# Kernel optimization log

Hardware: AMD Instinct MI355X
Metric: run time of the kernel (lower is better)

The kernel has to match this reference:

```python
import jax, jax.numpy as jnp
import numpy as np

B, I, HID, H, KS = 64, 1024, 2048, 8, 4
D = HID // H  # head_size = 256; also BlockDiagonal block size = (2*I)//H = 256
EPS = 1e-5


def setup_inputs() -> dict:
    key = jax.random.key(0)
    ks = jax.random.split(key, 16)
    r = lambda i, shape, s=0.02: jax.random.normal(ks[i], shape, dtype=jnp.float32) * s
    z = lambda shape: jnp.zeros(shape, jnp.float32)
    return {
        "x": jax.random.normal(ks[0], (B, I), dtype=jnp.float32),
        "h_prev": z((B, H, D)),
        "c_prev": z((B, H, D, D)),
        "n_prev": z((B, H, D)),
        "m_prev": z((B, H)),
        "ln_w": jnp.ones((I,), jnp.float32), "ln_b": z((I,)),
        "W_ul": r(1, (I, HID)), "b_ul": z((HID,)),
        "W_ur": r(2, (I, HID)), "b_ur": z((HID,)),
        "W_conv": r(3, (HID, HID, KS)), "b_conv": z((HID,)),
        "W_skip": r(4, (HID, HID)), "b_skip": z((HID,)),
        "W_q": r(5, (H, D, D)), "b_q": z((HID,)),
        "W_k": r(6, (H, D, D)), "b_k": z((HID,)),
        "W_v": r(7, (H, D, D)), "b_v": z((HID,)),
        "W_i": r(8, (HID, H)), "b_i": z((H,)),
        "W_f": r(9, (HID, H)), "b_f": z((H,)),
        "W_o": r(10, (HID, HID)), "b_o": z((HID,)),
        "W_down": r(11, (HID, I)), "b_down": z((I,)),
        "gn_w": jnp.ones((HID,), jnp.float32), "gn_b": z((HID,)),
    }


def _block_diag(zf, W, b):
    # BlockDiagonal: chunk last dim into H blocks, per-block Linear, concat -> [B,H,D]
    zh = zf.reshape(zf.shape[0], H, -1)
    return jnp.einsum('bhi,hio->bho', zh, W) + b.reshape(H, -1)


def reference(x, h_prev, c_prev, n_prev, m_prev, ln_w, ln_b, W_ul, b_ul, W_ur, b_ur,
              W_conv, b_conv, W_skip, b_skip, W_q, b_q, W_k, b_k, W_v, b_v,
              W_i, b_i, W_f, b_f, W_o, b_o, W_down, b_down, gn_w, gn_b):
    # LayerNorm
    mu = x.mean(-1, keepdims=True)
    var = jnp.mean((x - mu) ** 2, -1, keepdims=True)
    xn = (x - mu) * jax.lax.rsqrt(var + EPS) * ln_w + ln_b
    # Up projections
    xl = xn @ W_ul + b_ul            # [B, 2I] == [B, HID]
    xr = xn @ W_ur + b_ur
    # Causal conv over a length-1 sequence: after left padding + slicing, only the
    # last kernel tap (index KS-1) touches real data -> linear map with W_conv[:,:,KS-1]
    xc = jax.nn.silu(xl @ W_conv[:, :, KS - 1].T + b_conv)
    x_skip = xc @ W_skip + b_skip    # [B, HID]
    q = _block_diag(xc, W_q, b_q)                       # [B,H,D]
    k = _block_diag(xc, W_k, b_k) / jnp.sqrt(jnp.float32(D))
    v = _block_diag(xl, W_v, b_v)
    i_t = xc @ W_i + b_i             # [B,H]
    f_t = xc @ W_f + b_f
    o = jax.nn.sigmoid(xl @ W_o + b_o).reshape(-1, H, D)
    # Stabilized exponential gating
    m_t = jnp.maximum(f_t + m_prev, i_t)
    i_g = jnp.exp(i_t - m_t)
    f_g = jnp.exp(f_t + m_prev - m_t)
    # Outer-product state update + bilinear readout
    c_t = f_g[..., None, None] * c_prev + i_g[..., None, None] * jnp.einsum('bhd,bhk->bhdk', v, k)
    n_t = f_g[..., None] * n_prev + i_g[..., None] * k
    num = jnp.einsum('bhdk,bhk->bhd', c_t, q)
    den = jnp.clip(jnp.einsum('bhd,bhd->bh', n_t, q), 1.0, None)[..., None]
    h_t = o * num / den              # [B,H,D]
    # GroupNorm with num_groups == num_heads: normalize per head
    g_mu = h_t.mean(-1, keepdims=True)
    g_var = jnp.mean((h_t - g_mu) ** 2, -1, keepdims=True)
    gn = ((h_t - g_mu) * jax.lax.rsqrt(g_var + EPS)).reshape(-1, HID) * gn_w + gn_b
    out = (gn + x_skip) * jax.nn.silu(xr)
    out = out @ W_down + b_down
    final = out + x
    return (final, h_t, c_t, n_t, m_t)
```

## Files before the change

kernel.cpp:

```cpp
#include <hip/hip_runtime.h>
#include <cstddef>

typedef __bf16 bf16;
typedef __bf16 bf16x8 __attribute__((ext_vector_type(8)));
typedef short  s16x8  __attribute__((ext_vector_type(8)));
typedef float  f32x4  __attribute__((ext_vector_type(4)));

template <class T> T&& declv() noexcept;
template <class, class = void> struct takes_bf16vec { static constexpr bool value = false; };
template <class V> struct takes_bf16vec<V, decltype((void)__builtin_amdgcn_mfma_f32_16x16x32_bf16(
    declv<V>(), declv<V>(), declv<f32x4>(), 0, 0, 0))> { static constexpr bool value = true; };

template <class V>
__device__ __forceinline__ f32x4 mfma_bf16_16x16x32(V a, V b, f32x4 c) {
  if constexpr (takes_bf16vec<V>::value) {
    return __builtin_amdgcn_mfma_f32_16x16x32_bf16(a, b, c, 0, 0, 0);
  } else {
    return __builtin_amdgcn_mfma_f32_16x16x32_bf16(
        __builtin_bit_cast(s16x8, a), __builtin_bit_cast(s16x8, b), c, 0, 0, 0);
  }
}

constexpr int M_NONE = 0, M_SILU = 1, M_SIG = 2, M_SCALE = 3, M_FINAL = 4;
constexpr int FLAG_BD = 1, FLAG_S4 = 2;

__global__ __launch_bounds__(256) void ln_kernel(const float* __restrict__ x,
                                                 const float* __restrict__ w,
                                                 const float* __restrict__ bs,
                                                 bf16* __restrict__ xn) {
  const int b = blockIdx.x, tid = threadIdx.x;
  __shared__ float red[256];
  float vals[4];
  float s = 0.f;
#pragma unroll
  for (int i = 0; i < 4; ++i) { vals[i] = x[b * 1024 + i * 256 + tid]; s += vals[i]; }
  red[tid] = s; __syncthreads();
  for (int off = 128; off; off >>= 1) { if (tid < off) red[tid] += red[tid + off]; __syncthreads(); }
  const float mu = red[0] * (1.f / 1024.f);
  __syncthreads();
  float s2 = 0.f;
#pragma unroll
  for (int i = 0; i < 4; ++i) { const float d = vals[i] - mu; s2 += d * d; }
  red[tid] = s2; __syncthreads();
  for (int off = 128; off; off >>= 1) { if (tid < off) red[tid] += red[tid + off]; __syncthreads(); }
  const float rs = rsqrtf(red[0] * (1.f / 1024.f) + 1e-5f);
#pragma unroll
  for (int i = 0; i < 4; ++i) {
    const int j = i * 256 + tid;
    xn[b * 1024 + j] = (bf16)((vals[i] - mu) * rs * w[j] + bs[j]);
  }
}

__global__ __launch_bounds__(256) void gemm_sk(
    const bf16* __restrict__ A, const float* __restrict__ W,
    const float* __restrict__ bias, const float* __restrict__ xadd,
    float* __restrict__ outF, bf16* __restrict__ outB,
    int K, int N, int ldA, int mode, int flags) {
  const int tid = threadIdx.x;
  const int lane = tid & 63, wave = tid >> 6;
  const int l15 = lane & 15, quad = lane >> 4;
  const int n0 = blockIdx.x << 4;
  const bool bd = (flags & FLAG_BD) != 0, s4 = (flags & FLAG_S4) != 0;

  int Keff = K, aCol0 = 0, ldB = N, wn0 = n0;
  const float* Wb = W;
  if (bd) {
    const int h = n0 >> 8;
    Keff = 256; aCol0 = h << 8; Wb = W + (size_t)h * 65536; ldB = 256; wn0 = n0 & 255;
  }
  const int kchunk = Keff >> 2;
  const int kbeg = wave * kchunk, kend = kbeg + kchunk;

  f32x4 acc0{}, acc1{}, acc2{}, acc3{};
  for (int k = kbeg; k < kend; k += 32) {
    const int kk = k + quad * 8;
    bf16x8 bfrag;
    if (s4) {
      const float* wp = W + ((size_t)(wn0 + l15) * 2048 + kk) * 4 + 3;
#pragma unroll
      for (int j = 0; j < 8; ++j) bfrag[j] = (bf16)wp[j * 4];
    } else {
      const float* wp = Wb + (size_t)kk * ldB + wn0 + l15;
#pragma unroll
      for (int j = 0; j < 8; ++j) bfrag[j] = (bf16)wp[(size_t)j * ldB];
    }
    const bf16* ap = A + (size_t)l15 * ldA + aCol0 + kk;
    const size_t st = (size_t)16 * ldA;
    bf16x8 a0 = *(const bf16x8*)(ap);
    bf16x8 a1 = *(const bf16x8*)(ap + st);
    bf16x8 a2 = *(const bf16x8*)(ap + 2 * st);
    bf16x8 a3 = *(const bf16x8*)(ap + 3 * st);
    acc0 = mfma_bf16_16x16x32(a0, bfrag, acc0);
    acc1 = mfma_bf16_16x16x32(a1, bfrag, acc1);
    acc2 = mfma_bf16_16x16x32(a2, bfrag, acc2);
    acc3 = mfma_bf16_16x16x32(a3, bfrag, acc3);
  }
  __shared__ float lds[4][64][20];
#pragma unroll
  for (int r = 0; r < 4; ++r) {
    const int rr = quad * 4 + r;
    lds[wave][rr][l15]      = acc0[r];
    lds[wave][16 + rr][l15] = acc1[r];
    lds[wave][32 + rr][l15] = acc2[r];
    lds[wave][48 + rr][l15] = acc3[r];
  }
  __syncthreads();
  const int col = tid & 15, rb = (tid >> 4) << 2;
  const float bv = bias[n0 + col];
#pragma unroll
  for (int r2 = 0; r2 < 4; ++r2) {
    const int row = rb + r2;
    float v = lds[0][row][col] + lds[1][row][col] + lds[2][row][col] + lds[3][row][col] + bv;
    if (mode == M_SILU)       v = v / (1.f + expf(-v));
    else if (mode == M_SIG)   v = 1.f / (1.f + expf(-v));
    else if (mode == M_SCALE) v *= 0.0625f;
    else if (mode == M_FINAL) v += xadd[(size_t)row * N + n0 + col];
    const size_t oi = (size_t)row * N + n0 + col;
    if (outF) outF[oi] = v;
    if (outB) outB[oi] = (bf16)v;
  }
}

__global__ __launch_bounds__(256) void gates_kernel(
    const bf16* __restrict__ xc, const float* __restrict__ Wi, const float* __restrict__ bi,
    const float* __restrict__ Wf, const float* __restrict__ bfv, const float* __restrict__ m_prev,
    float* __restrict__ ig, float* __restrict__ fg, float* __restrict__ mt_out) {
  const int b = blockIdx.x, tid = threadIdx.x;
  float ai[8] = {}, af[8] = {};
  for (int k = tid; k < 2048; k += 256) {
    const float xv = (float)xc[b * 2048 + k];
    const float4 wi0 = *(const float4*)(Wi + (size_t)k * 8);
    const float4 wi1 = *(const float4*)(Wi + (size_t)k * 8 + 4);
    const float4 wf0 = *(const float4*)(Wf + (size_t)k * 8);
    const float4 wf1 = *(const float4*)(Wf + (size_t)k * 8 + 4);
    ai[0] += xv * wi0.x; ai[1] += xv * wi0.y; ai[2] += xv * wi0.z; ai[3] += xv * wi0.w;
    ai[4] += xv * wi1.x; ai[5] += xv * wi1.y; ai[6] += xv * wi1.z; ai[7] += xv * wi1.w;
    af[0] += xv * wf0.x; af[1] += xv * wf0.y; af[2] += xv * wf0.z; af[3] += xv * wf0.w;
    af[4] += xv * wf1.x; af[5] += xv * wf1.y; af[6] += xv * wf1.z; af[7] += xv * wf1.w;
  }
  __shared__ float ri[256][8], rf[256][8];
#pragma unroll
  for (int h = 0; h < 8; ++h) { ri[tid][h] = ai[h]; rf[tid][h] = af[h]; }
  __syncthreads();
  for (int off = 128; off; off >>= 1) {
    if (tid < off) {
#pragma unroll
      for (int h = 0; h < 8; ++h) { ri[tid][h] += ri[tid + off][h]; rf[tid][h] += rf[tid + off][h]; }
    }
    __syncthreads();
  }
  if (tid < 8) {
    const float it = ri[0][tid] + bi[tid];
    const float ft = rf[0][tid] + bfv[tid];
    const float mp = m_prev[b * 8 + tid];
    const float mt = fmaxf(ft + mp, it);
    mt_out[b * 8 + tid] = mt;
    ig[b * 8 + tid] = expf(it - mt);
    fg[b * 8 + tid] = expf(ft + mp - mt);
  }
}

__global__ __launch_bounds__(256) void state_kernel(
    const float* __restrict__ c_prev, const float* __restrict__ n_prev,
    const float* __restrict__ qf, const float* __restrict__ kf,
    const float* __restrict__ vf, const float* __restrict__ of,
    const float* __restrict__ ig, const float* __restrict__ fg,
    const float* __restrict__ xskip, const float* __restrict__ xrf,
    const float* __restrict__ gnw, const float* __restrict__ gnb,
    float* __restrict__ ct_out, float* __restrict__ nt_out,
    float* __restrict__ ht_out, bf16* __restrict__ pre_bf) {
  const int bh = blockIdx.x, b = bh >> 3, h = bh & 7;
  const int tid = threadIdx.x, lane = tid & 63, wave = tid >> 6;
  const int vb = b * 2048 + h * 256;

  __shared__ float q_s[256], k_s[256], v_s[256], num_s[256], red[256];

  const float i_g = ig[bh], f_g = fg[bh];
  const float kv = kf[vb + tid], qv = qf[vb + tid];
  q_s[tid] = qv; k_s[tid] = kv; v_s[tid] = vf[vb + tid];
  const float nv = f_g * n_prev[bh * 256 + tid] + i_g * kv;
  nt_out[bh * 256 + tid] = nv;
  red[tid] = nv * qv;
  __syncthreads();
  for (int off = 128; off; off >>= 1) { if (tid < off) red[tid] += red[tid + off]; __syncthreads(); }
  const float den = fmaxf(red[0], 1.0f);

  const size_t cb = (size_t)bh << 16;
  const int c0 = lane << 2;
  const float qx = q_s[c0], qy = q_s[c0 + 1], qz = q_s[c0 + 2], qw = q_s[c0 + 3];
  const float kx = k_s[c0], ky = k_s[c0 + 1], kz = k_s[c0 + 2], kw = k_s[c0 + 3];
  for (int r = 0; r < 64; ++r) {
    const int row = (wave << 6) + r;
    const float vd = v_s[row];
    const size_t off = cb + ((size_t)row << 8) + c0;
    const float4 cp = *(const float4*)(c_prev + off);
    float4 cn;
    cn.x = f_g * cp.x + i_g * kx * vd;
    cn.y = f_g * cp.y + i_g * ky * vd;
    cn.z = f_g * cp.z + i_g * kz * vd;
    cn.w = f_g * cp.w + i_g * kw * vd;
    *(float4*)(ct_out + off) = cn;
    float p = cn.x * qx + cn.y * qy + cn.z * qz + cn.w * qw;
#pragma unroll
    for (int m = 32; m; m >>= 1) p += __shfl_xor(p, m, 64);
    if (lane == 0) num_s[row] = p;
  }
  __syncthreads();

  const float num = num_s[tid];
  const float hv = of[vb + tid] * num / den;
  ht_out[bh * 256 + tid] = hv;

  __syncthreads();
  red[tid] = hv; __syncthreads();
  for (int off = 128; off; off >>= 1) { if (tid < off) red[tid] += red[tid + off]; __syncthreads(); }
  const float mu = red[0] * (1.f / 256.f);
  __syncthreads();
  const float dv = hv - mu;
  red[tid] = dv * dv; __syncthreads();
  for (int off = 128; off; off >>= 1) { if (tid < off) red[tid] += red[tid + off]; __syncthreads(); }
  const float gn = (hv - mu) * rsqrtf(red[0] * (1.f / 256.f) + 1e-5f);

  const int j = h * 256 + tid;
  const float xr = xrf[b * 2048 + j];
  const float pre = (gn * gnw[j] + gnb[j] + xskip[b * 2048 + j]) * (xr / (1.f + expf(-xr)));
  pre_bf[b * 2048 + j] = (bf16)pre;
}

extern "C" void kernel_launch(void* const* d_in, const int* in_sizes, int n_in,
                              void* d_out, int out_size, void* d_ws, size_t ws_size,
                              hipStream_t stream) {
  (void)in_sizes; (void)n_in; (void)out_size; (void)ws_size;
  const float* x      = (const float*)d_in[0];
  const float* c_prev = (const float*)d_in[2];
  const float* n_prev = (const float*)d_in[3];
  const float* m_prev = (const float*)d_in[4];
  const float* ln_w = (const float*)d_in[5];
  const float* ln_b = (const float*)d_in[6];
  const float* W_ul = (const float*)d_in[7];
  const float* b_ul = (const float*)d_in[8];
  const float* W_ur = (const float*)d_in[9];
  const float* b_ur = (const float*)d_in[10];
  const float* W_conv = (const float*)d_in[11];
  const float* b_conv = (const float*)d_in[12];
  const float* W_skip = (const float*)d_in[13];
  const float* b_skip = (const float*)d_in[14];
  const float* W_q = (const float*)d_in[15];
  const float* b_q = (const float*)d_in[16];
  const float* W_k = (const float*)d_in[17];
  const float* b_k = (const float*)d_in[18];
  const float* W_v = (const float*)d_in[19];
  const float* b_v = (const float*)d_in[20];
  const float* W_i = (const float*)d_in[21];
  const float* b_i = (const float*)d_in[22];
  const float* W_f = (const float*)d_in[23];
  const float* b_f = (const float*)d_in[24];
  const float* W_o = (const float*)d_in[25];
  const float* b_o = (const float*)d_in[26];
  const float* W_down = (const float*)d_in[27];
  const float* b_down = (const float*)d_in[28];
  const float* gn_w = (const float*)d_in[29];
  const float* gn_b = (const float*)d_in[30];

  float* out_final = (float*)d_out;
  float* out_ht = out_final + 65536;
  float* out_ct = out_final + 196608;
  float* out_nt = out_final + 33751040;
  float* out_mt = out_final + 33882112;

  char* ws = (char*)d_ws;
  bf16*  xn_bf   = (bf16*)(ws + 0);
  bf16*  xl_bf   = (bf16*)(ws + 131072);
  bf16*  xc_bf   = (bf16*)(ws + 393216);
  bf16*  pre_bf  = (bf16*)(ws + 655360);
  float* xr_f    = (float*)(ws + 917504);
  float* xskip_f = (float*)(ws + 1441792);
  float* q_f     = (float*)(ws + 1966080);
  float* k_f     = (float*)(ws + 2490368);
  float* v_f     = (float*)(ws + 3014656);
  float* o_f     = (float*)(ws + 3538944);
  float* ig_f    = (float*)(ws + 4063232);
  float* fg_f    = (float*)(ws + 4065280);

  ln_kernel<<<64, 256, 0, stream>>>(x, ln_w, ln_b, xn_bf);
  gemm_sk<<<128, 256, 0, stream>>>(xn_bf, W_ul, b_ul, nullptr, nullptr, xl_bf, 1024, 2048, 1024, M_NONE, 0);
  gemm_sk<<<128, 256, 0, stream>>>(xn_bf, W_ur, b_ur, nullptr, xr_f, nullptr, 1024, 2048, 1024, M_NONE, 0);
  gemm_sk<<<128, 256, 0, stream>>>(xl_bf, W_conv, b_conv, nullptr, nullptr, xc_bf, 2048, 2048, 2048, M_SILU, FLAG_S4);
  gemm_sk<<<128, 256, 0, stream>>>(xc_bf, W_skip, b_skip, nullptr, xskip_f, nullptr, 2048, 2048, 2048, M_NONE, 0);
  gemm_sk<<<128, 256, 0, stream>>>(xc_bf, W_q, b_q, nullptr, q_f, nullptr, 256, 2048, 2048, M_NONE, FLAG_BD);
  gemm_sk<<<128, 256, 0, stream>>>(xc_bf, W_k, b_k, nullptr, k_f, nullptr, 256, 2048, 2048, M_SCALE, FLAG_BD);
  gemm_sk<<<128, 256, 0, stream>>>(xl_bf, W_v, b_v, nullptr, v_f, nullptr, 256, 2048, 2048, M_NONE, FLAG_BD);
  gemm_sk<<<128, 256, 0, stream>>>(xl_bf, W_o, b_o, nullptr, o_f, nullptr, 2048, 2048, 2048, M_SIG, 0);
  gates_kernel<<<64, 256, 0, stream>>>(xc_bf, W_i, b_i, W_f, b_f, m_prev, ig_f, fg_f, out_mt);
  state_kernel<<<512, 256, 0, stream>>>(c_prev, n_prev, q_f, k_f, v_f, o_f, ig_f, fg_f,
                                        xskip_f, xr_f, gn_w, gn_b, out_ct, out_nt, out_ht, pre_bf);
  gemm_sk<<<64, 256, 0, stream>>>(pre_bf, W_down, b_down, x, out_final, nullptr, 2048, 1024, 2048, M_FINAL, 0);
}
```

Measured before the change: 521.8 us.

## Split-K GEMMs with combine kernels, merge paired projections, split state update

Projection GEMMs now use split-K with templated compile-time sizes, writing partial sums that a separate combine kernel reduces and then applies bias and activation. Paired GEMMs that share inputs (ul/ur, skip/o) are merged into one launch, and the q/k/v block-diagonal GEMMs are fused into a single launch. The state update is split into a kernel with 4096 blocks that streams c_prev and a second kernel for normalization, which raises parallelism beyond the earlier 128 or 512 blocks. Output buffers (c_t and h_t) are reused as scratch for the partial sums, and the extra launches and partial-sum traffic add cost.

Result: faster. 448.8 us (-14.0%).

```diff
diff --git a/kernel.cpp b/kernel.cpp
--- a/kernel.cpp
+++ b/kernel.cpp
@@ -22,7 +22,6 @@
 }
 
 constexpr int M_NONE = 0, M_SILU = 1, M_SIG = 2, M_SCALE = 3, M_FINAL = 4;
-constexpr int FLAG_BD = 1, FLAG_S4 = 2;
 
 __global__ __launch_bounds__(256) void ln_kernel(const float* __restrict__ x,
                                                  const float* __restrict__ w,
@@ -51,40 +50,46 @@
   }
 }
 
-__global__ __launch_bounds__(256) void gemm_sk(
-    const bf16* __restrict__ A, const float* __restrict__ W,
-    const float* __restrict__ bias, const float* __restrict__ xadd,
-    float* __restrict__ outF, bf16* __restrict__ outB,
-    int K, int N, int ldA, int mode, int flags) {
+template <int K, int KS, int NTILES, bool S4, bool DUAL>
+__global__ __launch_bounds__(256) void gemm_part(
+    const bf16* __restrict__ A0, const bf16* __restrict__ A1,
+    const float* __restrict__ W0, const float* __restrict__ W1,
+    int ldA, int ldB, float* __restrict__ part) {
+  constexpr int Ncomb = NTILES * 16;
+  constexpr int Kslice = K / KS;
+  constexpr int chunk = Kslice / 4;
   const int tid = threadIdx.x;
   const int lane = tid & 63, wave = tid >> 6;
   const int l15 = lane & 15, quad = lane >> 4;
-  const int n0 = blockIdx.x << 4;
-  const bool bd = (flags & FLAG_BD) != 0, s4 = (flags & FLAG_S4) != 0;
-
-  int Keff = K, aCol0 = 0, ldB = N, wn0 = n0;
-  const float* Wb = W;
-  if (bd) {
-    const int h = n0 >> 8;
-    Keff = 256; aCol0 = h << 8; Wb = W + (size_t)h * 65536; ldB = 256; wn0 = n0 & 255;
-  }
-  const int kchunk = Keff >> 2;
-  const int kbeg = wave * kchunk, kend = kbeg + kchunk;
+  const int tile = blockIdx.x % NTILES, ks = blockIdx.x / NTILES;
+
+  const bf16* A = A0;
+  const float* W = W0;
+  int ncol;
+  if (DUAL) {
+    const int seg = tile >> 7;
+    if (seg) { A = A1; W = W1; }
+    ncol = (tile & 127) * 16;
+  } else {
+    ncol = tile * 16;
+  }
+  const int kbeg = ks * Kslice + wave * chunk;
 
   f32x4 acc0{}, acc1{}, acc2{}, acc3{};
-  for (int k = kbeg; k < kend; k += 32) {
-    const int kk = k + quad * 8;
+#pragma unroll
+  for (int k = 0; k < chunk; k += 32) {
+    const int kk = kbeg + k + quad * 8;
     bf16x8 bfrag;
-    if (s4) {
-      const float* wp = W + ((size_t)(wn0 + l15) * 2048 + kk) * 4 + 3;
+    if (S4) {
+      const float* wp = W + ((size_t)(ncol + l15) * 2048 + kk) * 4 + 3;
 #pragma unroll
       for (int j = 0; j < 8; ++j) bfrag[j] = (bf16)wp[j * 4];
     } else {
-      const float* wp = Wb + (size_t)kk * ldB + wn0 + l15;
+      const float* wp = W + (size_t)kk * ldB + ncol + l15;
 #pragma unroll
       for (int j = 0; j < 8; ++j) bfrag[j] = (bf16)wp[(size_t)j * ldB];
     }
-    const bf16* ap = A + (size_t)l15 * ldA + aCol0 + kk;
+    const bf16* ap = A + (size_t)l15 * ldA + kk;
     const size_t st = (size_t)16 * ldA;
     bf16x8 a0 = *(const bf16x8*)(ap);
     bf16x8 a1 = *(const bf16x8*)(ap + st);
@@ -106,15 +111,157 @@
   }
   __syncthreads();
   const int col = tid & 15, rb = (tid >> 4) << 2;
+#pragma unroll
+  for (int r2 = 0; r2 < 4; ++r2) {
+    const int row = rb + r2;
+    const float v = lds[0][row][col] + lds[1][row][col] + lds[2][row][col] + lds[3][row][col];
+    part[((size_t)ks * 64 + row) * Ncomb + tile * 16 + col] = v;
+  }
+}
+
+__global__ __launch_bounds__(256) void combine(
+    const float* __restrict__ part, int KS, int Ncomb, int halfN,
+    const float* __restrict__ bias0, const float* __restrict__ bias1,
+    int mode0, int mode1,
+    float* __restrict__ outF0, bf16* __restrict__ outB0,
+    float* __restrict__ outF1, bf16* __restrict__ outB1,
+    const float* __restrict__ xadd) {
+  const int e = (blockIdx.x * 256 + threadIdx.x) * 4;
+  const int total = 64 * Ncomb;
+  if (e >= total) return;
+  const int row = e / Ncomb, col = e - row * Ncomb;
+  float4 s = *(const float4*)(part + e);
+  for (int ks = 1; ks < KS; ++ks) {
+    const float4 p = *(const float4*)(part + (size_t)ks * total + e);
+    s.x += p.x; s.y += p.y; s.z += p.z; s.w += p.w;
+  }
+  const int seg = (col >= halfN) ? 1 : 0;
+  const int cn = col - seg * halfN;
+  const float* bias = seg ? bias1 : bias0;
+  const int mode = seg ? mode1 : mode0;
+  float* outF = seg ? outF1 : outF0;
+  bf16* outB = seg ? outB1 : outB0;
+  float vv[4] = {s.x, s.y, s.z, s.w};
+#pragma unroll
+  for (int j = 0; j < 4; ++j) {
+    float v = vv[j] + bias[cn + j];
+    if (mode == M_SILU)       v = v / (1.f + expf(-v));
+    else if (mode == M_SIG)   v = 1.f / (1.f + expf(-v));
+    else if (mode == M_SCALE) v *= 0.0625f;
+    else if (mode == M_FINAL) v += xadd[(size_t)row * halfN + cn + j];
+    const size_t oi = (size_t)row * halfN + cn + j;
+    if (outF) outF[oi] = v;
+    if (outB) outB[oi] = (bf16)v;
+  }
+}
+
+__global__ __launch_bounds__(256) void gemm_qkv(
+    const bf16* __restrict__ xc, const bf16* __restrict__ xl,
+    const float* __restrict__ Wq, const float* __restrict__ bq,
+    const float* __restrict__ Wk, const float* __restrict__ bk,
+    const float* __restrict__ Wv, const float* __restrict__ bv,
+    float* __restrict__ qf, float* __restrict__ kf, float* __restrict__ vf) {
+  const int tid = threadIdx.x;
+  const int lane = tid & 63, wave = tid >> 6;
+  const int l15 = lane & 15, quad = lane >> 4;
+  const int seg = blockIdx.x >> 7, t = blockIdx.x & 127;
+  const int n0 = t * 16, h = t >> 4, wn0 = n0 & 255;
+  const bf16* A = (seg == 2) ? xl : xc;
+  const float* W = (seg == 0) ? Wq : (seg == 1) ? Wk : Wv;
+  const float* bias = (seg == 0) ? bq : (seg == 1) ? bk : bv;
+  float* out = (seg == 0) ? qf : (seg == 1) ? kf : vf;
+  const float* Wb = W + (size_t)h * 65536;
+  const int aCol0 = h << 8;
+  const int kbeg = wave * 64;
+
+  f32x4 acc0{}, acc1{}, acc2{}, acc3{};
+#pragma unroll
+  for (int k = 0; k < 64; k += 32) {
+    const int kk = kbeg + k + quad * 8;
+    bf16x8 bfrag;
+    const float* wp = Wb + (size_t)kk * 256 + wn0 + l15;
+#pragma unroll
+    for (int j = 0; j < 8; ++j) bfrag[j] = (bf16)wp[(size_t)j * 256];
+    const bf16* ap = A + (size_t)l15 * 2048 + aCol0 + kk;
+    const size_t st = (size_t)16 * 2048;
+    bf16x8 a0 = *(const bf16x8*)(ap);
+    bf16x8 a1 = *(const bf16x8*)(ap + st);
+    bf16x8 a2 = *(const bf16x8*)(ap + 2 * st);
+    bf16x8 a3 = *(const bf16x8*)(ap + 3 * st);
+    acc0 = mfma_bf16_16x16x32(a0, bfrag, acc0);
+    acc1 = mfma_bf16_16x16x32(a1, bfrag, acc1);
+    acc2 = mfma_bf16_16x16x32(a2, bfrag, acc2);
+    acc3 = mfma_bf16_16x16x32(a3, bfrag, acc3);
+  }
+  __shared__ float lds[4][64][20];
+#pragma unroll
+  for (int r = 0; r < 4; ++r) {
+    const int rr = quad * 4 + r;
+    lds[wave][rr][l15]      = acc0[r];
+    lds[wave][16 + rr][l15] = acc1[r];
+    lds[wave][32 + rr][l15] = acc2[r];
+    lds[wave][48 + rr][l15] = acc3[r];
+  }
+  __syncthreads();
+  const int col = tid & 15, rb = (tid >> 4) << 2;
+  const float bv_ = bias[n0 + col];
+#pragma unroll
+  for (int r2 = 0; r2 < 4; ++r2) {
+    const int row = rb + r2;
+    float v = lds[0][row][col] + lds[1][row][col] + lds[2][row][col] + lds[3][row][col] + bv_;
+    if (seg == 1) v *= 0.0625f;
+    out[(size_t)row * 2048 + n0 + col] = v;
+  }
+}
+
+__global__ __launch_bounds__(256) void gemm_sk(
+    const bf16* __restrict__ A, const float* __restrict__ W,
+    const float* __restrict__ bias, const float* __restrict__ xadd,
+    float* __restrict__ outF, bf16* __restrict__ outB,
+    int K, int N, int ldA, int mode) {
+  const int tid = threadIdx.x;
+  const int lane = tid & 63, wave = tid >> 6;
+  const int l15 = lane & 15, quad = lane >> 4;
+  const int n0 = blockIdx.x << 4;
+  const int ldB = N;
+  const int kchunk = K >> 2;
+  const int kbeg = wave * kchunk, kend = kbeg + kchunk;
+
+  f32x4 acc0{}, acc1{}, acc2{}, acc3{};
+  for (int k = kbeg; k < kend; k += 32) {
+    const int kk = k + quad * 8;
+    bf16x8 bfrag;
+    const float* wp = W + (size_t)kk * ldB + n0 + l15;
+#pragma unroll
+    for (int j = 0; j < 8; ++j) bfrag[j] = (bf16)wp[(size_t)j * ldB];
+    const bf16* ap = A + (size_t)l15 * ldA + kk;
+    const size_t st = (size_t)16 * ldA;
+    bf16x8 a0 = *(const bf16x8*)(ap);
+    bf16x8 a1 = *(const bf16x8*)(ap + st);
+    bf16x8 a2 = *(const bf16x8*)(ap + 2 * st);
+    bf16x8 a3 = *(const bf16x8*)(ap + 3 * st);
+    acc0 = mfma_bf16_16x16x32(a0, bfrag, acc0);
+    acc1 = mfma_bf16_16x16x32(a1, bfrag, acc1);
+    acc2 = mfma_bf16_16x16x32(a2, bfrag, acc2);
+    acc3 = mfma_bf16_16x16x32(a3, bfrag, acc3);
+  }
+  __shared__ float lds[4][64][20];
+#pragma unroll
+  for (int r = 0; r < 4; ++r) {
+    const int rr = quad * 4 + r;
+    lds[wave][rr][l15]      = acc0[r];
+    lds[wave][16 + rr][l15] = acc1[r];
+    lds[wave][32 + rr][l15] = acc2[r];
+    lds[wave][48 + rr][l15] = acc3[r];
+  }
+  __syncthreads();
+  const int col = tid & 15, rb = (tid >> 4) << 2;
   const float bv = bias[n0 + col];
 #pragma unroll
   for (int r2 = 0; r2 < 4; ++r2) {
     const int row = rb + r2;
     float v = lds[0][row][col] + lds[1][row][col] + lds[2][row][col] + lds[3][row][col] + bv;
-    if (mode == M_SILU)       v = v / (1.f + expf(-v));
-    else if (mode == M_SIG)   v = 1.f / (1.f + expf(-v));
-    else if (mode == M_SCALE) v *= 0.0625f;
-    else if (mode == M_FINAL) v += xadd[(size_t)row * N + n0 + col];
+    if (mode == M_FINAL) v += xadd[(size_t)row * N + n0 + col];
     const size_t oi = (size_t)row * N + n0 + col;
     if (outF) outF[oi] = v;
     if (outB) outB[oi] = (bf16)v;
@@ -160,57 +307,65 @@
   }
 }
 
-__global__ __launch_bounds__(256) void state_kernel(
-    const float* __restrict__ c_prev, const float* __restrict__ n_prev,
-    const float* __restrict__ qf, const float* __restrict__ kf,
-    const float* __restrict__ vf, const float* __restrict__ of,
+__global__ __launch_bounds__(256) void state1(
+    const float* __restrict__ c_prev, const float* __restrict__ qf,
+    const float* __restrict__ kf, const float* __restrict__ vf,
     const float* __restrict__ ig, const float* __restrict__ fg,
-    const float* __restrict__ xskip, const float* __restrict__ xrf,
-    const float* __restrict__ gnw, const float* __restrict__ gnb,
-    float* __restrict__ ct_out, float* __restrict__ nt_out,
-    float* __restrict__ ht_out, bf16* __restrict__ pre_bf) {
+    float* __restrict__ ct_out, float* __restrict__ numw) {
+  const int bh = blockIdx.x >> 3, rg = blockIdx.x & 7;
+  const int tid = threadIdx.x;
+  const int b = bh >> 3, h = bh & 7, vb = b * 2048 + h * 256;
+  __shared__ float q_s[256], k_s[256];
+  q_s[tid] = qf[vb + tid];
+  k_s[tid] = kf[vb + tid];
+  __syncthreads();
+  const float i_g = ig[bh], f_g = fg[bh];
+  const int row = rg * 32 + (tid >> 3);
+  const int lane8 = tid & 7;
+  const float vd = vf[vb + row];
+  const float iv = i_g * vd;
+  const size_t base = ((size_t)bh << 16) + ((size_t)row << 8) + lane8 * 4;
+  float p = 0.f;
+#pragma unroll
+  for (int i = 0; i < 8; ++i) {
+    const int c = lane8 * 4 + i * 32;
+    const float4 cp = *(const float4*)(c_prev + base + i * 32);
+    float4 cn;
+    cn.x = f_g * cp.x + iv * k_s[c];
+    cn.y = f_g * cp.y + iv * k_s[c + 1];
+    cn.z = f_g * cp.z + iv * k_s[c + 2];
+    cn.w = f_g * cp.w + iv * k_s[c + 3];
+    *(float4*)(ct_out + base + i * 32) = cn;
+    p += cn.x * q_s[c] + cn.y * q_s[c + 1] + cn.z * q_s[c + 2] + cn.w * q_s[c + 3];
+  }
+#pragma unroll
+  for (int m = 1; m < 8; m <<= 1) p += __shfl_xor(p, m, 64);
+  if (lane8 == 0) numw[bh * 256 + row] = p;
+}
+
+__global__ __launch_bounds__(256) void state2(
+    const float* __restrict__ n_prev, const float* __restrict__ qf,
+    const float* __restrict__ kf, const float* __restrict__ of,
+    const float* __restrict__ ig, const float* __restrict__ fg,
+    const float* numw, const float* __restrict__ xskip,
+    const float* __restrict__ xrf, const float* __restrict__ gnw,
+    const float* __restrict__ gnb, float* __restrict__ nt_out,
+    float* ht_out, bf16* __restrict__ pre_bf) {
   const int bh = blockIdx.x, b = bh >> 3, h = bh & 7;
-  const int tid = threadIdx.x, lane = tid & 63, wave = tid >> 6;
+  const int tid = threadIdx.x;
   const int vb = b * 2048 + h * 256;
-
-  __shared__ float q_s[256], k_s[256], v_s[256], num_s[256], red[256];
-
+  __shared__ float red[256];
   const float i_g = ig[bh], f_g = fg[bh];
-  const float kv = kf[vb + tid], qv = qf[vb + tid];
-  q_s[tid] = qv; k_s[tid] = kv; v_s[tid] = vf[vb + tid];
+  const float qv = qf[vb + tid], kv = kf[vb + tid];
   const float nv = f_g * n_prev[bh * 256 + tid] + i_g * kv;
   nt_out[bh * 256 + tid] = nv;
   red[tid] = nv * qv;
   __syncthreads();
   for (int off = 128; off; off >>= 1) { if (tid < off) red[tid] += red[tid + off]; __syncthreads(); }
   const float den = fmaxf(red[0], 1.0f);
-
-  const size_t cb = (size_t)bh << 16;
-  const int c0 = lane << 2;
-  const float qx = q_s[c0], qy = q_s[c0 + 1], qz = q_s[c0 + 2], qw = q_s[c0 + 3];
-  const float kx = k_s[c0], ky = k_s[c0 + 1], kz = k_s[c0 + 2], kw = k_s[c0 + 3];
-  for (int r = 0; r < 64; ++r) {
-    const int row = (wave << 6) + r;
-    const float vd = v_s[row];
-    const size_t off = cb + ((size_t)row << 8) + c0;
-    const float4 cp = *(const float4*)(c_prev + off);
-    float4 cn;
-    cn.x = f_g * cp.x + i_g * kx * vd;
-    cn.y = f_g * cp.y + i_g * ky * vd;
-    cn.z = f_g * cp.z + i_g * kz * vd;
-    cn.w = f_g * cp.w + i_g * kw * vd;
-    *(float4*)(ct_out + off) = cn;
-    float p = cn.x * qx + cn.y * qy + cn.z * qz + cn.w * qw;
-#pragma unroll
-    for (int m = 32; m; m >>= 1) p += __shfl_xor(p, m, 64);
-    if (lane == 0) num_s[row] = p;
-  }
-  __syncthreads();
-
-  const float num = num_s[tid];
+  const float num = numw[bh * 256 + tid];
   const float hv = of[vb + tid] * num / den;
   ht_out[bh * 256 + tid] = hv;
-
   __syncthreads();
   red[tid] = hv; __syncthreads();
   for (int off = 128; off; off >>= 1) { if (tid < off) red[tid] += red[tid + off]; __syncthreads(); }
@@ -220,7 +375,6 @@
   red[tid] = dv * dv; __syncthreads();
   for (int off = 128; off; off >>= 1) { if (tid < off) red[tid] += red[tid + off]; __syncthreads(); }
   const float gn = (hv - mu) * rsqrtf(red[0] * (1.f / 256.f) + 1e-5f);
-
   const int j = h * 256 + tid;
   const float xr = xrf[b * 2048 + j];
   const float pre = (gn * gnw[j] + gnb[j] + xskip[b * 2048 + j]) * (xr / (1.f + expf(-xr)));
@@ -281,18 +435,28 @@
   float* o_f     = (float*)(ws + 3538944);
   float* ig_f    = (float*)(ws + 4063232);
   float* fg_f    = (float*)(ws + 4065280);
+  float* num_f   = out_ht;
+  float* part    = out_ct;
 
   ln_kernel<<<64, 256, 0, stream>>>(x, ln_w, ln_b, xn_bf);
-  gemm_sk<<<128, 256, 0, stream>>>(xn_bf, W_ul, b_ul, nullptr, nullptr, xl_bf, 1024, 2048, 1024, M_NONE, 0);
-  gemm_sk<<<128, 256, 0, stream>>>(xn_bf, W_ur, b_ur, nullptr, xr_f, nullptr, 1024, 2048, 1024, M_NONE, 0);
-  gemm_sk<<<128, 256, 0, stream>>>(xl_bf, W_conv, b_conv, nullptr, nullptr, xc_bf, 2048, 2048, 2048, M_SILU, FLAG_S4);
-  gemm_sk<<<128, 256, 0, stream>>>(xc_bf, W_skip, b_skip, nullptr, xskip_f, nullptr, 2048, 2048, 2048, M_NONE, 0);
-  gemm_sk<<<128, 256, 0, stream>>>(xc_bf, W_q, b_q, nullptr, q_f, nullptr, 256, 2048, 2048, M_NONE, FLAG_BD);
-  gemm_sk<<<128, 256, 0, stream>>>(xc_bf, W_k, b_k, nullptr, k_f, nullptr, 256, 2048, 2048, M_SCALE, FLAG_BD);
-  gemm_sk<<<128, 256, 0, stream>>>(xl_bf, W_v, b_v, nullptr, v_f, nullptr, 256, 2048, 2048, M_NONE, FLAG_BD);
-  gemm_sk<<<128, 256, 0, stream>>>(xl_bf, W_o, b_o, nullptr, o_f, nullptr, 2048, 2048, 2048, M_SIG, 0);
+  gemm_part<1024, 4, 256, false, true><<<1024, 256, 0, stream>>>(
+      xn_bf, xn_bf, W_ul, W_ur, 1024, 2048, part);
+  combine<<<256, 256, 0, stream>>>(part, 4, 4096, 2048, b_ul, b_ur, M_NONE, M_NONE,
+                                   nullptr, xl_bf, xr_f, nullptr, nullptr);
+  gemm_part<2048, 8, 128, true, false><<<1024, 256, 0, stream>>>(
+      xl_bf, nullptr, W_conv, nullptr, 2048, 2048, part);
+  combine<<<128, 256, 0, stream>>>(part, 8, 2048, 2048, b_conv, nullptr, M_SILU, M_NONE,
+                                   nullptr, xc_bf, nullptr, nullptr, nullptr);
+  gemm_part<2048, 4, 256, false, true><<<1024, 256, 0, stream>>>(
+      xc_bf, xl_bf, W_skip, W_o, 2048, 2048, part);
+  combine<<<256, 256, 0, stream>>>(part, 4, 4096, 2048, b_skip, b_o, M_NONE, M_SIG,
+                                   xskip_f, nullptr, o_f, nullptr, nullptr);
+  gemm_qkv<<<384, 256, 0, stream>>>(xc_bf, xl_bf, W_q, b_q, W_k, b_k, W_v, b_v,
+                                    q_f, k_f, v_f);
   gates_kernel<<<64, 256, 0, stream>>>(xc_bf, W_i, b_i, W_f, b_f, m_prev, ig_f, fg_f, out_mt);
-  state_kernel<<<512, 256, 0, stream>>>(c_prev, n_prev, q_f, k_f, v_f, o_f, ig_f, fg_f,
-                                        xskip_f, xr_f, gn_w, gn_b, out_ct, out_nt, out_ht, pre_bf);
-  gemm_sk<<<64, 256, 0, stream>>>(pre_bf, W_down, b_down, x, out_final, nullptr, 2048, 1024, 2048, M_FINAL, 0);
-}
+  state1<<<4096, 256, 0, stream>>>(c_prev, q_f, k_f, v_f, ig_f, fg_f, out_ct, num_f);
+  state2<<<512, 256, 0, stream>>>(n_prev, q_f, k_f, o_f, ig_f, fg_f, num_f,
+                                  xskip_f, xr_f, gn_w, gn_b, out_nt, out_ht, pre_bf);
+  gemm_sk<<<64, 256, 0, stream>>>(pre_bf, W_down, b_down, x, out_final, nullptr,
+                                  2048, 1024, 2048, M_FINAL);
+}
```
